# Optimization experiments

Hardware: AMD Instinct MI355X
Metric: run time of the kernel (lower is better)

Reference implementation:

```python
import jax, jax.numpy as jnp
import numpy as np

B, T, C, H = 4, 2048, 1024, 16
D = C // H  # head dim = 64

def precompute_rope(dim, max_pos):
    # rope_cache[t, i] = (cos(t*theta_i), sin(t*theta_i)), theta_i = 10000^(-2i/dim)
    i = jnp.arange(dim // 2, dtype=jnp.float32)
    theta = 1.0 / (10000.0 ** (2.0 * i / dim))
    t = jnp.arange(max_pos, dtype=jnp.float32)[:, None]
    ang = t * theta[None, :]
    return jnp.stack([jnp.cos(ang), jnp.sin(ang)], axis=-1)  # (max_pos, dim/2, 2)

def apply_rope(x, rope):
    # x: (B, H, T, D); complex multiply rope * x over pairs of channels
    Tq = x.shape[2]
    xr = x.reshape(x.shape[0], x.shape[1], Tq, D // 2, 2)
    a, b = xr[..., 0], xr[..., 1]
    c = rope[:Tq, :, 0]  # (T, D/2)
    s = rope[:Tq, :, 1]
    real = a * c - b * s
    imag = a * s + b * c
    return jnp.stack([real, imag], axis=-1).reshape(x.shape)

def setup_inputs() -> dict:
    key = jax.random.key(0)
    ks = jax.random.split(key, 9)
    scale = 1.0 / np.sqrt(C)
    def w(k):
        return jax.random.uniform(k, (C, C), jnp.float32, -scale, scale)
    def bvec(k):
        return jax.random.uniform(k, (C,), jnp.float32, -scale, scale)
    return {
        "x": jax.random.normal(ks[0], (B, T, C), jnp.float32),
        "Wq": w(ks[1]), "bq": bvec(ks[2]),
        "Wk": w(ks[3]), "bk": bvec(ks[4]),
        "Wv": w(ks[5]), "bv": bvec(ks[6]),
        "Wp": w(ks[7]), "bp": bvec(ks[8]),
        "rope_cache": precompute_rope(D, T),
    }

def reference(x, Wq, bq, Wk, bk, Wv, bv, Wp, bp, rope_cache):
    B_, T_, C_ = x.shape
    def heads(y):
        return y.reshape(B_, T_, H, D).transpose(0, 2, 1, 3)  # (B,H,T,D)
    q = heads(x @ Wq.T + bq)
    k = heads(x @ Wk.T + bk)
    v = heads(x @ Wv.T + bv)
    q = apply_rope(q, rope_cache)
    k = apply_rope(k, rope_cache)
    att = jnp.einsum("bhqd,bhkd->bhqk", q, k) * (1.0 / np.sqrt(D))
    causal = jnp.tril(jnp.ones((T_, T_), dtype=bool))
    att = jnp.where(causal, att, jnp.float32(-1e10))
    att = jax.nn.softmax(att, axis=-1)
    y = jnp.einsum("bhqk,bhkd->bhqd", att, v)
    y = y.transpose(0, 2, 1, 3).reshape(B_, T_, C_)
    return y @ Wp.T + bp
```

## Files before the change

kernel.cpp:

```cpp
#include <hip/hip_runtime.h>

#define DEVINL __device__ __forceinline__

typedef unsigned short u16;
typedef __attribute__((ext_vector_type(4))) short s16x4;
typedef __attribute__((ext_vector_type(8))) short s16x8;
typedef __attribute__((ext_vector_type(4))) float f32x4;

static constexpr int Bb = 4, Tt = 2048, Cc = 1024, Hh = 16, Dd = 64;
static constexpr int Mm = Bb * Tt;
static constexpr int KK = Cc;

DEVINL float bf2f(u16 u) { return __uint_as_float(((unsigned)u) << 16); }
DEVINL u16 f2bf(float f) {
  unsigned b = __float_as_uint(f);
  b += 0x7fff + ((b >> 16) & 1);
  return (u16)(b >> 16);
}
DEVINL unsigned cvtpk(float lo, float hi) {
  unsigned r;
  asm("v_cvt_pk_bf16_f32 %0, %1, %2" : "=v"(r) : "v"(lo), "v"(hi));
  return r;
}

#define GLDS(gsrc, ldst) \
  __builtin_amdgcn_global_load_lds((const __attribute__((address_space(1))) void*)(gsrc), \
                                   (__attribute__((address_space(3))) void*)(ldst), 16, 0, 0)

struct Cvt5Args { const float* s[5]; u16* d[5]; int n4[5]; };
__global__ void cvt5(Cvt5Args a) {
  const int y = blockIdx.y;
  const float* __restrict__ src = a.s[y];
  u16* __restrict__ dst = a.d[y];
  const int n4 = a.n4[y];
  int i = blockIdx.x * blockDim.x + threadIdx.x;
  int st = gridDim.x * blockDim.x;
  for (int g = i; g < n4; g += st) {
    float4 v = ((const float4*)src)[g];
    uint2 o;
    o.x = (unsigned)f2bf(v.x) | ((unsigned)f2bf(v.y) << 16);
    o.y = (unsigned)f2bf(v.z) | ((unsigned)f2bf(v.w) << 16);
    ((uint2*)dst)[g] = o;
  }
}

#define GEMM_PROLOG()                                              \
  const int tid = threadIdx.x, w = tid >> 6, l = tid & 63;         \
  const int lr = l & 15, lg = l >> 4;                              \
  const int m0 = blockIdx.x * 128, n0 = blockIdx.y * 128;          \
  const int wr = w >> 1, wc = w & 1;                               \
  f32x4 zero = {0.f, 0.f, 0.f, 0.f};                               \
  f32x4 acc[4][4];                                                 \
  _Pragma("unroll") for (int i = 0; i < 4; ++i)                    \
      _Pragma("unroll") for (int j = 0; j < 4; ++j) acc[i][j] = zero; \
  const int srow = l >> 3;                                         \
  const int scolsw = ((l & 7) ^ (l >> 3)) * 8;

#define GEMM_STAGE(Aptr, Wptr, k0, buf)                                                  \
  _Pragma("unroll") for (int i = 0; i < 4; ++i) {                                        \
    int row = i * 32 + w * 8 + srow;                                                     \
    GLDS(Aptr + (size_t)(m0 + row) * KK + (k0) + scolsw, &As[buf][(i * 32 + w * 8) * 64]); \
    GLDS(Wptr + (size_t)(n0 + row) * KK + (k0) + scolsw, &Bs[buf][(i * 32 + w * 8) * 64]); \
  }

#define GEMM_KLOOP_DB(Aptr, Wptr)                                                        \
  GEMM_STAGE(Aptr, Wptr, 0, 0)                                                           \
  for (int k0 = 0; k0 < KK; k0 += 64) {                                                  \
    const int buf = (k0 >> 6) & 1;                                                       \
    if (k0 + 64 < KK) {                                                                  \
      GEMM_STAGE(Aptr, Wptr, k0 + 64, buf ^ 1)                                           \
      asm volatile("s_waitcnt vmcnt(8)" ::: "memory");            \
    } else {                                                                             \
      asm volatile("s_waitcnt vmcnt(0)" ::: "memory");                                   \
    }                                                                                    \
    __builtin_amdgcn_s_barrier();                                                        \
    __builtin_amdgcn_sched_barrier(0);                                                   \
    _Pragma("unroll") for (int kk = 0; kk < 2; ++kk) {                                   \
      s16x8 af[4], bfr[4];                                                               \
      _Pragma("unroll") for (int i = 0; i < 4; ++i)                                      \
          af[i] = *(const s16x8*)&As[buf][(wr * 64 + i * 16 + lr) * 64 +                 \
                                         ((kk * 32 + lg * 8) ^ ((lr & 7) << 3))];        \
      _Pragma("unroll") for (int j = 0; j < 4; ++j)                                      \
          bfr[j] = *(const s16x8*)&Bs[buf][(wc * 64 + j * 16 + lr) * 64 +                \
                                          ((kk * 32 + lg * 8) ^ ((lr & 7) << 3))];       \
      _Pragma("unroll") for (int i = 0; i < 4; ++i)                                      \
          _Pragma("unroll") for (int j = 0; j < 4; ++j)                                  \
              acc[i][j] =                                                                \
                  __builtin_amdgcn_mfma_f32_16x16x32_bf16(af[i], bfr[j], acc[i][j], 0, 0, 0); \
    }                                                                                    \
    __builtin_amdgcn_sched_barrier(0);                                                   \
    __builtin_amdgcn_s_barrier();       \
  }

__global__ __launch_bounds__(256) void gemm_qk(const u16* __restrict__ A,
                                               const u16* __restrict__ W0,
                                               const u16* __restrict__ W1,
                                               const float* __restrict__ b0,
                                               const float* __restrict__ b1,
                                               const float* __restrict__ rope,
                                               u16* __restrict__ O0, u16* __restrict__ O1) {
  __shared__ __align__(16) u16 As[2][128 * 64];
  __shared__ __align__(16) u16 Bs[2][128 * 64];
  const int z = blockIdx.z;
  const u16* __restrict__ Wt = z ? W1 : W0;
  const float* __restrict__ bias = z ? b1 : b0;
  u16* __restrict__ O = z ? O1 : O0;
  const float scl = z ? 1.0f : 0.18033688f;
  GEMM_PROLOG()
  GEMM_KLOOP_DB(A, Wt)
#pragma unroll
  for (int j = 0; j < 4; ++j) {
    int ncol = n0 + wc * 64 + j * 16 + lr;
    float bj = bias[ncol];
    int hh = ncol >> 6, dd = ncol & 63;
    const float sign = (dd & 1) ? 1.0f : -1.0f;
    const float* csp = rope + (dd >> 1) * 2;
#pragma unroll
    for (int i = 0; i < 4; ++i) {
#pragma unroll
      for (int r = 0; r < 4; ++r) {
        int mrow = m0 + wr * 64 + i * 16 + lg * 4 + r;
        int bb2 = mrow >> 11, tt2 = mrow & (Tt - 1);
        float v = acc[i][j][r] + bj;
        float part = __shfl_xor(v, 1);
        float2 cs = *(const float2*)(csp + tt2 * 64);
        float outv = (v * cs.x + sign * part * cs.y) * scl;
        O[(((size_t)bb2 * Hh + hh) * Tt + tt2) * Dd + dd] = f2bf(outv);
      }
    }
  }
}

__global__ __launch_bounds__(256) void gemm_v(const u16* __restrict__ A,
                                              const u16* __restrict__ Wt,
                                              const float* __restrict__ bias,
                                              u16* __restrict__ O) {
  __shared__ __align__(16) u16 As[2][128 * 64];
  __shared__ __align__(16) u16 Bs[2][128 * 64];
  __shared__ __align__(16) u16 Ts[128 * 64];
  GEMM_PROLOG()
  GEMM_KLOOP_DB(A, Wt)
  const int bb2 = m0 >> 11, tloc = m0 & (Tt - 1);
#pragma unroll
  for (int p = 0; p < 2; ++p) {
    if (p) __syncthreads();
    if (wr == p) {
#pragma unroll
      for (int j = 0; j < 4; ++j) {
        int ncl = wc * 64 + j * 16 + lr;
        float bj = bias[n0 + ncl];
        int xw = (ncl & 3) << 2;
#pragma unroll
        for (int i = 0; i < 4; ++i) {
          s16x4 pk;
#pragma unroll
          for (int r = 0; r < 4; ++r) pk[r] = (short)f2bf(acc[i][j][r] + bj);
          *(s16x4*)&Ts[ncl * 64 + (((i * 4 + lg) ^ xw) << 2)] = pk;
        }
      }
    }
    __syncthreads();
    const int rn = tid >> 3, t8 = tid & 7;
#pragma unroll
    for (int it = 0; it < 4; ++it) {
      int rown = it * 32 + rn;
      int slot = (t8 * 2) ^ ((rown & 3) << 2);
      s16x8 v = *(const s16x8*)&Ts[rown * 64 + slot * 4];
      int ncol = n0 + rown;
      int hh2 = ncol >> 6, dd = ncol & 63;
      *(s16x8*)&O[(((size_t)bb2 * Hh + hh2) * Dd + dd) * Tt + tloc + p * 64 + t8 * 8] = v;
    }
  }
}

__global__ __launch_bounds__(256) void gemm_proj(const u16* __restrict__ A,
                                                 const u16* __restrict__ Wt,
                                                 const float* __restrict__ bias,
                                                 float* __restrict__ O) {
  __shared__ __align__(16) u16 As[2][128 * 64];
  __shared__ __align__(16) u16 Bs[2][128 * 64];
  GEMM_PROLOG()
  GEMM_KLOOP_DB(A, Wt)
#pragma unroll
  for (int j = 0; j < 4; ++j) {
    int ncol = n0 + wc * 64 + j * 16 + lr;
    float bj = bias[ncol];
#pragma unroll
    for (int i = 0; i < 4; ++i) {
#pragma unroll
      for (int r = 0; r < 4; ++r) {
        int mrow = m0 + wr * 64 + i * 16 + lg * 4 + r;
        O[(size_t)mrow * Cc + ncol] = acc[i][j][r] + bj;
      }
    }
  }
}

__global__ __launch_bounds__(512, 8) void attn_kernel(const u16* __restrict__ Q,
                                                      const u16* __restrict__ K,
                                                      const u16* __restrict__ VTg,
                                                      u16* __restrict__ Out) {
  __shared__ __align__(16) u16 Ks[2][64 * 64];
  __shared__ __align__(16) u16 VTs[2][64 * 64];
  __shared__ __align__(16) u16 Ps[8 * 16 * 32];
  const int tid = threadIdx.x, w = tid >> 6, l = tid & 63;
  const int lr = l & 15, lg = l >> 4;
  const int wq = w & 3;
  const int n = blockIdx.x + 16 * blockIdx.y;
  const int bh = ((n & 7) << 3) + (n >> 7);
  const int qt = (n >> 3) & 15;
  const int qtH = 31 - qt;
  const int myqt = (w < 4) ? qtH : qt;
  const size_t base = (size_t)bh * Tt * Dd;
  const u16* Qp = Q + base;
  const u16* Kp = K + base;
  const u16* Vp = VTg + base;
  const int bb2 = bh >> 4, hh = bh & 15;
  const float NEG = -3.0e9f;
  f32x4 zero = {0.f, 0.f, 0.f, 0.f};
  const int krow_l = l >> 3, kc8sw = ((l & 7) ^ (l >> 3)) * 8;
  const int psw = (lr >> 1) & 3;

  const int qg = myqt * 64 + wq * 16 + lr;
  s16x8 qf[2];
  qf[0] = *(const s16x8*)(Qp + (size_t)qg * 64 + lg * 8);
  qf[1] = *(const s16x8*)(Qp + (size_t)qg * 64 + 32 + lg * 8);
  f32x4 o[4] = {zero, zero, zero, zero};
  float m = -3e38f, lsum = 0.f;

  auto stage = [&](int kt, int buf) {
    const int kk0 = kt * 64;
    int row = w * 8 + krow_l;
    GLDS(Kp + (size_t)(kk0 + row) * 64 + kc8sw, &Ks[buf][(w * 8) * 64]);
    GLDS(Vp + (size_t)row * Tt + kk0 + kc8sw, &VTs[buf][(w * 8) * 64]);
  };

  const int htiles = qtH + 1;
  stage(0, 0);
  for (int kt = 0; kt < htiles; ++kt) {
    const int buf = kt & 1;
    if (kt + 1 < htiles) {
      stage(kt + 1, buf ^ 1);
      asm volatile("s_waitcnt vmcnt(2)" ::: "memory");
    } else {
      asm volatile("s_waitcnt vmcnt(0)" ::: "memory");
    }
    __builtin_amdgcn_s_barrier();
    __builtin_amdgcn_sched_barrier(0);
    if (w < 4 || kt <= qt) {
      float pv[4][4];
      const int diag = (kt == myqt);
      __builtin_amdgcn_s_setprio(1);
#pragma unroll
      for (int cf = 0; cf < 4; ++cf) {
        f32x4 s = zero;
#pragma unroll
        for (int kf = 0; kf < 2; ++kf) {
          s16x8 kb = *(const s16x8*)&Ks[buf][(cf * 16 + lr) * 64 +
                                            (((kf * 4 + lg) ^ (lr & 7)) << 3)];
          s = __builtin_amdgcn_mfma_f32_16x16x32_bf16(kb, qf[kf], s, 0, 0, 0);
        }
        if (diag) {
          int key0 = kt * 64 + cf * 16 + lg * 4;
#pragma unroll
          for (int r = 0; r < 4; ++r) pv[cf][r] = (key0 + r <= qg) ? s[r] : NEG;
        } else {
#pragma unroll
          for (int r = 0; r < 4; ++r) pv[cf][r] = s[r];
        }
      }
      __builtin_amdgcn_s_setprio(0);
      float t0 = fmaxf(fmaxf(pv[0][0], pv[0][1]), fmaxf(pv[0][2], pv[0][3]));
#pragma unroll
      for (int cf = 1; cf < 4; ++cf) {
        float tc = fmaxf(fmaxf(pv[cf][0], pv[cf][1]), fmaxf(pv[cf][2], pv[cf][3]));
        t0 = fmaxf(t0, tc);
      }
      if (!__all(t0 <= m + 11.5f)) {
        float t1 = fmaxf(t0, __shfl_xor(t0, 16));
        float tm = fmaxf(t1, __shfl_xor(t1, 32));
        float mn = fmaxf(m, tm);
        float fsc = __builtin_amdgcn_exp2f(m - mn);
        lsum *= fsc;
        m = mn;
#pragma unroll
        for (int jf = 0; jf < 4; ++jf) {
          o[jf][0] *= fsc; o[jf][1] *= fsc; o[jf][2] *= fsc; o[jf][3] *= fsc;
        }
      }
      float psum = 0.f;
#pragma unroll
      for (int cf = 0; cf < 4; ++cf)
#pragma unroll
        for (int r = 0; r < 4; ++r) {
          float p = __builtin_amdgcn_exp2f(pv[cf][r] - m);
          pv[cf][r] = p;
          psum += p;
        }
      lsum += psum;
#pragma unroll
      for (int kk = 0; kk < 2; ++kk) {
#pragma unroll
        for (int c = 0; c < 2; ++c) {
          int cf = kk * 2 + c;
          unsigned w0 = cvtpk(pv[cf][0], pv[cf][1]);
          unsigned w1 = cvtpk(pv[cf][2], pv[cf][3]);
          int col0 = c * 16 + lg * 4;
          int idx = w * 512 + lr * 32 + ((((col0 >> 3) ^ psw)) << 3) + (col0 & 7);
          *(unsigned*)&Ps[idx] = w0;
          *(unsigned*)&Ps[idx + 2] = w1;
        }
        s16x8 pa = *(const s16x8*)&Ps[w * 512 + lr * 32 + ((lg ^ psw) << 3)];
        __builtin_amdgcn_s_setprio(1);
#pragma unroll
        for (int jf = 0; jf < 4; ++jf) {
          s16x8 vb = *(const s16x8*)&VTs[buf][(jf * 16 + lr) * 64 +
                                             (((kk * 4 + lg) ^ (lr & 7)) << 3)];
          o[jf] = __builtin_amdgcn_mfma_f32_16x16x32_bf16(vb, pa, o[jf], 0, 0, 0);
        }
        __builtin_amdgcn_s_setprio(0);
      }
    }
    __builtin_amdgcn_sched_barrier(0);
    __builtin_amdgcn_s_barrier();
  }
  lsum += __shfl_xor(lsum, 16);
  lsum += __shfl_xor(lsum, 32);
  float linv = 1.0f / lsum;
  u16* orow = Out + ((size_t)(bb2 * Tt + qg)) * Cc + hh * 64 + lg * 4;
#pragma unroll
  for (int jf = 0; jf < 4; ++jf) {
    uint2 pk;
    pk.x = cvtpk(o[jf][0] * linv, o[jf][1] * linv);
    pk.y = cvtpk(o[jf][2] * linv, o[jf][3] * linv);
    *(uint2*)&orow[jf * 16] = pk;
  }
}

extern "C" void kernel_launch(void* const* d_in, const int* in_sizes, int n_in,
                              void* d_out, int out_size, void* d_ws, size_t ws_size,
                              hipStream_t stream) {
  (void)in_sizes; (void)n_in; (void)out_size; (void)ws_size;
  const float* x = (const float*)d_in[0];
  const float* Wq = (const float*)d_in[1];
  const float* bq = (const float*)d_in[2];
  const float* Wk = (const float*)d_in[3];
  const float* bk = (const float*)d_in[4];
  const float* Wv = (const float*)d_in[5];
  const float* bv = (const float*)d_in[6];
  const float* Wp = (const float*)d_in[7];
  const float* bp = (const float*)d_in[8];
  const float* rope = (const float*)d_in[9];

  char* ws = (char*)d_ws;
  const size_t MB = 1024 * 1024;
  u16* xb  = (u16*)(ws + 0);
  u16* wqb = (u16*)(ws + 16 * MB);
  u16* wkb = (u16*)(ws + 18 * MB);
  u16* wvb = (u16*)(ws + 20 * MB);
  u16* wpb = (u16*)(ws + 22 * MB);
  u16* qb  = (u16*)(ws + 24 * MB);
  u16* kb  = (u16*)(ws + 40 * MB);
  u16* vt  = (u16*)(ws + 56 * MB);
  u16* att = (u16*)(ws + 72 * MB);

  Cvt5Args ca;
  ca.s[0] = x;  ca.d[0] = xb;  ca.n4[0] = (Mm * Cc) / 4;
  ca.s[1] = Wq; ca.d[1] = wqb; ca.n4[1] = (Cc * Cc) / 4;
  ca.s[2] = Wk; ca.d[2] = wkb; ca.n4[2] = (Cc * Cc) / 4;
  ca.s[3] = Wv; ca.d[3] = wvb; ca.n4[3] = (Cc * Cc) / 4;
  ca.s[4] = Wp; ca.d[4] = wpb; ca.n4[4] = (Cc * Cc) / 4;
  cvt5<<<dim3(512, 5), 256, 0, stream>>>(ca);

  gemm_qk<<<dim3(Mm / 128, Cc / 128, 2), 256, 0, stream>>>(xb, wqb, wkb, bq, bk, rope, qb, kb);
  gemm_v<<<dim3(Mm / 128, Cc / 128), 256, 0, stream>>>(xb, wvb, bv, vt);

  attn_kernel<<<dim3(16, Bb * Hh), 512, 0, stream>>>(qb, kb, vt, att);

  gemm_proj<<<dim3(Mm / 128, Cc / 128), 256, 0, stream>>>(att, wpb, bp, (float*)d_out);
}
```

Before: 177.6 us.

## Process four query tiles per attention block with 32 rows per wave

Each attention block now covers four query tiles (two pairs balanced for causal work) instead of two. Each wave handles 32 query rows in two 16-row sub-tiles, so every K and V fragment read from LDS feeds two MFMAs and each K/V tile staged into LDS serves more queries. The grid is halved and launch bounds are lowered to allow more registers. The cost is higher register pressure, fewer blocks in flight, and idle waves on the shorter tiles while the block iterates to the longest one.

Result: no change. 180.0 us (+1.3%).

```diff
diff --git a/kernel.cpp b/kernel.cpp
--- a/kernel.cpp
+++ b/kernel.cpp
@@ -196,21 +196,20 @@
   }
 }
 
-__global__ __launch_bounds__(512, 8) void attn_kernel(const u16* __restrict__ Q,
+__global__ __launch_bounds__(512, 4) void attn_kernel(const u16* __restrict__ Q,
                                                       const u16* __restrict__ K,
                                                       const u16* __restrict__ VTg,
                                                       u16* __restrict__ Out) {
   __shared__ __align__(16) u16 Ks[2][64 * 64];
   __shared__ __align__(16) u16 VTs[2][64 * 64];
-  __shared__ __align__(16) u16 Ps[8 * 16 * 32];
+  __shared__ __align__(16) u16 Ps[8 * 2 * 16 * 32];
   const int tid = threadIdx.x, w = tid >> 6, l = tid & 63;
   const int lr = l & 15, lg = l >> 4;
-  const int wq = w & 3;
-  const int n = blockIdx.x + 16 * blockIdx.y;
-  const int bh = ((n & 7) << 3) + (n >> 7);
-  const int qt = (n >> 3) & 15;
-  const int qtH = 31 - qt;
-  const int myqt = (w < 4) ? qtH : qt;
+  const int n = blockIdx.x + 8 * blockIdx.y;
+  const int bh = ((n & 7) << 3) | (n >> 6);
+  const int pp = (n >> 3) & 7;
+  const int tsel = w >> 1, half = w & 1;
+  const int myqt = (tsel == 0) ? 31 - pp : (tsel == 1) ? 16 + pp : (tsel == 2) ? 15 - pp : pp;
   const size_t base = (size_t)bh * Tt * Dd;
   const u16* Qp = Q + base;
   const u16* Kp = K + base;
@@ -221,12 +220,20 @@
   const int krow_l = l >> 3, kc8sw = ((l & 7) ^ (l >> 3)) * 8;
   const int psw = (lr >> 1) & 3;
 
-  const int qg = myqt * 64 + wq * 16 + lr;
-  s16x8 qf[2];
-  qf[0] = *(const s16x8*)(Qp + (size_t)qg * 64 + lg * 8);
-  qf[1] = *(const s16x8*)(Qp + (size_t)qg * 64 + 32 + lg * 8);
-  f32x4 o[4] = {zero, zero, zero, zero};
-  float m = -3e38f, lsum = 0.f;
+  const int qbase = myqt * 64 + half * 32;
+  s16x8 qf[2][2];
+#pragma unroll
+  for (int qs = 0; qs < 2; ++qs) {
+    const u16* qp = Qp + (size_t)(qbase + qs * 16 + lr) * 64;
+    qf[qs][0] = *(const s16x8*)(qp + lg * 8);
+    qf[qs][1] = *(const s16x8*)(qp + 32 + lg * 8);
+  }
+  f32x4 o[2][4];
+#pragma unroll
+  for (int qs = 0; qs < 2; ++qs)
+#pragma unroll
+    for (int jf = 0; jf < 4; ++jf) o[qs][jf] = zero;
+  float m[2] = {-3e38f, -3e38f}, lsum[2] = {0.f, 0.f};
 
   auto stage = [&](int kt, int buf) {
     const int kk0 = kt * 64;
@@ -235,7 +242,7 @@
     GLDS(Vp + (size_t)row * Tt + kk0 + kc8sw, &VTs[buf][(w * 8) * 64]);
   };
 
-  const int htiles = qtH + 1;
+  const int htiles = 32 - pp;
   stage(0, 0);
   for (int kt = 0; kt < htiles; ++kt) {
     const int buf = kt & 1;
@@ -247,76 +254,90 @@
     }
     __builtin_amdgcn_s_barrier();
     __builtin_amdgcn_sched_barrier(0);
-    if (w < 4 || kt <= qt) {
-      float pv[4][4];
+    if (kt <= myqt) {
+      float pv[2][4][4];
       const int diag = (kt == myqt);
       __builtin_amdgcn_s_setprio(1);
 #pragma unroll
       for (int cf = 0; cf < 4; ++cf) {
-        f32x4 s = zero;
+        f32x4 s0 = zero, s1 = zero;
 #pragma unroll
         for (int kf = 0; kf < 2; ++kf) {
           s16x8 kb = *(const s16x8*)&Ks[buf][(cf * 16 + lr) * 64 +
                                             (((kf * 4 + lg) ^ (lr & 7)) << 3)];
-          s = __builtin_amdgcn_mfma_f32_16x16x32_bf16(kb, qf[kf], s, 0, 0, 0);
+          s0 = __builtin_amdgcn_mfma_f32_16x16x32_bf16(kb, qf[0][kf], s0, 0, 0, 0);
+          s1 = __builtin_amdgcn_mfma_f32_16x16x32_bf16(kb, qf[1][kf], s1, 0, 0, 0);
         }
         if (diag) {
           int key0 = kt * 64 + cf * 16 + lg * 4;
 #pragma unroll
-          for (int r = 0; r < 4; ++r) pv[cf][r] = (key0 + r <= qg) ? s[r] : NEG;
+          for (int r = 0; r < 4; ++r) {
+            pv[0][cf][r] = (key0 + r <= qbase + lr) ? s0[r] : NEG;
+            pv[1][cf][r] = (key0 + r <= qbase + 16 + lr) ? s1[r] : NEG;
+          }
         } else {
 #pragma unroll
-          for (int r = 0; r < 4; ++r) pv[cf][r] = s[r];
+          for (int r = 0; r < 4; ++r) { pv[0][cf][r] = s0[r]; pv[1][cf][r] = s1[r]; }
         }
       }
       __builtin_amdgcn_s_setprio(0);
-      float t0 = fmaxf(fmaxf(pv[0][0], pv[0][1]), fmaxf(pv[0][2], pv[0][3]));
-#pragma unroll
-      for (int cf = 1; cf < 4; ++cf) {
-        float tc = fmaxf(fmaxf(pv[cf][0], pv[cf][1]), fmaxf(pv[cf][2], pv[cf][3]));
-        t0 = fmaxf(t0, tc);
-      }
-      if (!__all(t0 <= m + 11.5f)) {
-        float t1 = fmaxf(t0, __shfl_xor(t0, 16));
-        float tm = fmaxf(t1, __shfl_xor(t1, 32));
-        float mn = fmaxf(m, tm);
-        float fsc = __builtin_amdgcn_exp2f(m - mn);
-        lsum *= fsc;
-        m = mn;
-#pragma unroll
-        for (int jf = 0; jf < 4; ++jf) {
-          o[jf][0] *= fsc; o[jf][1] *= fsc; o[jf][2] *= fsc; o[jf][3] *= fsc;
-        }
-      }
-      float psum = 0.f;
-#pragma unroll
-      for (int cf = 0; cf < 4; ++cf)
-#pragma unroll
-        for (int r = 0; r < 4; ++r) {
-          float p = __builtin_amdgcn_exp2f(pv[cf][r] - m);
-          pv[cf][r] = p;
-          psum += p;
-        }
-      lsum += psum;
+#pragma unroll
+      for (int qs = 0; qs < 2; ++qs) {
+        float t0 = fmaxf(fmaxf(pv[qs][0][0], pv[qs][0][1]), fmaxf(pv[qs][0][2], pv[qs][0][3]));
+#pragma unroll
+        for (int cf = 1; cf < 4; ++cf) {
+          float tc = fmaxf(fmaxf(pv[qs][cf][0], pv[qs][cf][1]),
+                           fmaxf(pv[qs][cf][2], pv[qs][cf][3]));
+          t0 = fmaxf(t0, tc);
+        }
+        if (!__all(t0 <= m[qs] + 11.5f)) {
+          float t1 = fmaxf(t0, __shfl_xor(t0, 16));
+          float tm = fmaxf(t1, __shfl_xor(t1, 32));
+          float mn = fmaxf(m[qs], tm);
+          float fsc = __builtin_amdgcn_exp2f(m[qs] - mn);
+          lsum[qs] *= fsc;
+          m[qs] = mn;
+#pragma unroll
+          for (int jf = 0; jf < 4; ++jf) {
+            o[qs][jf][0] *= fsc; o[qs][jf][1] *= fsc;
+            o[qs][jf][2] *= fsc; o[qs][jf][3] *= fsc;
+          }
+        }
+        float psum = 0.f;
+#pragma unroll
+        for (int cf = 0; cf < 4; ++cf)
+#pragma unroll
+          for (int r = 0; r < 4; ++r) {
+            float p = __builtin_amdgcn_exp2f(pv[qs][cf][r] - m[qs]);
+            pv[qs][cf][r] = p;
+            psum += p;
+          }
+        lsum[qs] += psum;
+      }
 #pragma unroll
       for (int kk = 0; kk < 2; ++kk) {
 #pragma unroll
-        for (int c = 0; c < 2; ++c) {
-          int cf = kk * 2 + c;
-          unsigned w0 = cvtpk(pv[cf][0], pv[cf][1]);
-          unsigned w1 = cvtpk(pv[cf][2], pv[cf][3]);
-          int col0 = c * 16 + lg * 4;
-          int idx = w * 512 + lr * 32 + ((((col0 >> 3) ^ psw)) << 3) + (col0 & 7);
-          *(unsigned*)&Ps[idx] = w0;
-          *(unsigned*)&Ps[idx + 2] = w1;
-        }
-        s16x8 pa = *(const s16x8*)&Ps[w * 512 + lr * 32 + ((lg ^ psw) << 3)];
+        for (int qs = 0; qs < 2; ++qs) {
+#pragma unroll
+          for (int c = 0; c < 2; ++c) {
+            int cf = kk * 2 + c;
+            unsigned w0 = cvtpk(pv[qs][cf][0], pv[qs][cf][1]);
+            unsigned w1 = cvtpk(pv[qs][cf][2], pv[qs][cf][3]);
+            int col0 = c * 16 + lg * 4;
+            int idx = w * 1024 + qs * 512 + lr * 32 + ((((col0 >> 3) ^ psw)) << 3) + (col0 & 7);
+            *(unsigned*)&Ps[idx] = w0;
+            *(unsigned*)&Ps[idx + 2] = w1;
+          }
+        }
+        s16x8 pa0 = *(const s16x8*)&Ps[w * 1024 + lr * 32 + ((lg ^ psw) << 3)];
+        s16x8 pa1 = *(const s16x8*)&Ps[w * 1024 + 512 + lr * 32 + ((lg ^ psw) << 3)];
         __builtin_amdgcn_s_setprio(1);
 #pragma unroll
         for (int jf = 0; jf < 4; ++jf) {
           s16x8 vb = *(const s16x8*)&VTs[buf][(jf * 16 + lr) * 64 +
                                              (((kk * 4 + lg) ^ (lr & 7)) << 3)];
-          o[jf] = __builtin_amdgcn_mfma_f32_16x16x32_bf16(vb, pa, o[jf], 0, 0, 0);
+          o[0][jf] = __builtin_amdgcn_mfma_f32_16x16x32_bf16(vb, pa0, o[0][jf], 0, 0, 0);
+          o[1][jf] = __builtin_amdgcn_mfma_f32_16x16x32_bf16(vb, pa1, o[1][jf], 0, 0, 0);
         }
         __builtin_amdgcn_s_setprio(0);
       }
@@ -324,16 +345,21 @@
     __builtin_amdgcn_sched_barrier(0);
     __builtin_amdgcn_s_barrier();
   }
-  lsum += __shfl_xor(lsum, 16);
-  lsum += __shfl_xor(lsum, 32);
-  float linv = 1.0f / lsum;
-  u16* orow = Out + ((size_t)(bb2 * Tt + qg)) * Cc + hh * 64 + lg * 4;
-#pragma unroll
-  for (int jf = 0; jf < 4; ++jf) {
-    uint2 pk;
-    pk.x = cvtpk(o[jf][0] * linv, o[jf][1] * linv);
-    pk.y = cvtpk(o[jf][2] * linv, o[jf][3] * linv);
-    *(uint2*)&orow[jf * 16] = pk;
+#pragma unroll
+  for (int qs = 0; qs < 2; ++qs) {
+    float ls = lsum[qs];
+    ls += __shfl_xor(ls, 16);
+    ls += __shfl_xor(ls, 32);
+    float linv = 1.0f / ls;
+    int tq = qbase + qs * 16 + lr;
+    u16* orow = Out + ((size_t)(bb2 * Tt + tq)) * Cc + hh * 64 + lg * 4;
+#pragma unroll
+    for (int jf = 0; jf < 4; ++jf) {
+      uint2 pk;
+      pk.x = cvtpk(o[qs][jf][0] * linv, o[qs][jf][1] * linv);
+      pk.y = cvtpk(o[qs][jf][2] * linv, o[qs][jf][3] * linv);
+      *(uint2*)&orow[jf * 16] = pk;
+    }
   }
 }
 
@@ -375,7 +401,7 @@
   gemm_qk<<<dim3(Mm / 128, Cc / 128, 2), 256, 0, stream>>>(xb, wqb, wkb, bq, bk, rope, qb, kb);
   gemm_v<<<dim3(Mm / 128, Cc / 128), 256, 0, stream>>>(xb, wvb, bv, vt);
 
-  attn_kernel<<<dim3(16, Bb * Hh), 512, 0, stream>>>(qb, kb, vt, att);
+  attn_kernel<<<dim3(8, Bb * Hh), 512, 0, stream>>>(qb, kb, vt, att);
 
   gemm_proj<<<dim3(Mm / 128, Cc / 128), 256, 0, stream>>>(att, wpb, bp, (float*)d_out);
 }
```
